# Kernel optimization log

Measured on AMD Instinct MI355X. Metric: run time of the kernel, lower is better.

Reference implementation:

```python
import jax, jax.numpy as jnp
import numpy as np
from jax import lax

HIDDEN = 1024; HEADS = 16; HEAD = 64; LAYERS = 4; MLP = 4096
PATCH = 16; TUBE = 2; CROP = 224; FRAMES = 16
GRID = CROP // PATCH          # 14
DEPTH = FRAMES // TUBE        # 8
N_TOK = DEPTH * GRID * GRID   # 1568
EPS = 1e-6
D_ROT = 2 * ((HEAD // 3) // 2)  # 20 per rotary axis (d, h, w); 4 dims left unrotated


def setup_inputs() -> dict:
    key = jax.random.key(0)
    ks = jax.random.split(key, 12)
    w = lambda k, shape: jax.random.normal(k, shape, jnp.float32) * 0.02
    L, H, M = LAYERS, HIDDEN, MLP
    return {
        "pixel_values_videos": jax.random.normal(ks[0], (2, FRAMES, 3, CROP, CROP), jnp.float32),
        "patch_w": w(ks[1], (H, 3, TUBE, PATCH, PATCH)),  # Conv3d OIDHW
        "patch_b": jnp.zeros((H,), jnp.float32),
        "ln1_g": jnp.ones((L, H), jnp.float32), "ln1_b": jnp.zeros((L, H), jnp.float32),
        "qw": w(ks[2], (L, H, H)), "qb": jnp.zeros((L, H), jnp.float32),
        "kw": w(ks[3], (L, H, H)), "kb": jnp.zeros((L, H), jnp.float32),
        "vw": w(ks[4], (L, H, H)), "vb": jnp.zeros((L, H), jnp.float32),
        "pw": w(ks[5], (L, H, H)), "pb": jnp.zeros((L, H), jnp.float32),
        "ln2_g": jnp.ones((L, H), jnp.float32), "ln2_b": jnp.zeros((L, H), jnp.float32),
        "fc1w": w(ks[6], (L, M, H)), "fc1b": jnp.zeros((L, M), jnp.float32),
        "fc2w": w(ks[7], (L, H, M)), "fc2b": jnp.zeros((L, H), jnp.float32),
        "lnf_g": jnp.ones((H,), jnp.float32), "lnf_b": jnp.zeros((H,), jnp.float32),
    }


def _layer_norm(x, g, b):
    mu = jnp.mean(x, axis=-1, keepdims=True)
    var = jnp.mean(jnp.square(x - mu), axis=-1, keepdims=True)
    return (x - mu) * lax.rsqrt(var + EPS) * g + b


def _position_ids():
    ids = jnp.arange(N_TOK)
    tpf = GRID * GRID
    d_pos = ids // tpf
    rem = ids - d_pos * tpf
    h_pos = rem // GRID
    w_pos = rem - h_pos * GRID
    return d_pos, h_pos, w_pos


def _rotate(x, pos):
    # x: (B, H, N, D); matches VJEPA2 rotate_queries_or_keys:
    # tiled (not interleaved) sin/cos * interleaved rotate-half.
    D = x.shape[-1]
    omega = 1.0 / (10000.0 ** (jnp.arange(D // 2, dtype=x.dtype) / (D / 2.0)))
    freq = pos.astype(x.dtype)[:, None] * omega              # (N, D/2)
    sin = jnp.concatenate([jnp.sin(freq)] * 2, axis=-1)      # (N, D) tiled (torch .repeat)
    cos = jnp.concatenate([jnp.cos(freq)] * 2, axis=-1)
    y = x.reshape(x.shape[:-1] + (D // 2, 2))
    y = jnp.stack([-y[..., 1], y[..., 0]], axis=-1).reshape(x.shape)
    return x * cos + y * sin


def _apply_rope(x, pos_ids):
    d_pos, h_pos, w_pos = pos_ids
    s0, s1, s2 = 0, D_ROT, 2 * D_ROT
    parts = [_rotate(x[..., s0:s1], d_pos), _rotate(x[..., s1:s2], h_pos),
             _rotate(x[..., s2:3 * D_ROT], w_pos)]
    if 3 * D_ROT < HEAD:
        parts.append(x[..., 3 * D_ROT:])
    return jnp.concatenate(parts, axis=-1)


def _forward(pixel_values_videos, patch_w, patch_b, ln1_g, ln1_b, qw, qb, kw, kb,
             vw, vb, pw, pb, ln2_g, ln2_b, fc1w, fc1b, fc2w, fc2b, lnf_g, lnf_b):
    B = pixel_values_videos.shape[0]
    x = jnp.transpose(pixel_values_videos, (0, 2, 1, 3, 4))  # (B, C, T, H, W)
    h = lax.conv_general_dilated(x, patch_w, window_strides=(TUBE, PATCH, PATCH),
                                 padding="VALID",
                                 dimension_numbers=("NCDHW", "OIDHW", "NCDHW"))
    h = h + patch_b[None, :, None, None, None]
    h = h.reshape(B, HIDDEN, -1).transpose(0, 2, 1)          # (B, N, HIDDEN)

    pos_ids = _position_ids()
    scale = HEAD ** -0.5

    for i in range(LAYERS):
        # attention block
        xn = _layer_norm(h, ln1_g[i], ln1_b[i])
        def heads(w_, b_):
            return (xn @ w_.T + b_).reshape(B, N_TOK, HEADS, HEAD).transpose(0, 2, 1, 3)
        q = _apply_rope(heads(qw[i], qb[i]), pos_ids)
        k = _apply_rope(heads(kw[i], kb[i]), pos_ids)
        v = heads(vw[i], vb[i])
        aw = jnp.einsum("bhnd,bhmd->bhnm", q, k) * scale
        aw = jax.nn.softmax(aw.astype(jnp.float32), axis=-1).astype(q.dtype)
        o = jnp.einsum("bhnm,bhmd->bhnd", aw, v)
        o = o.transpose(0, 2, 1, 3).reshape(B, N_TOK, HIDDEN)
        h = h + (o @ pw[i].T + pb[i])
        # MLP block
        xn = _layer_norm(h, ln2_g[i], ln2_b[i])
        m = jax.nn.gelu(xn @ fc1w[i].T + fc1b[i], approximate=False)
        h = h + (m @ fc2w[i].T + fc2b[i])

    return _layer_norm(h, lnf_g, lnf_b)


def reference(pixel_values_videos, patch_w, patch_b, ln1_g, ln1_b, qw, qb, kw, kb,
              vw, vb, pw, pb, ln2_g, ln2_b, fc1w, fc1b, fc2w, fc2b, lnf_g, lnf_b):
    return _forward(pixel_values_videos, patch_w, patch_b, ln1_g, ln1_b, qw, qb, kw, kb,
                    vw, vb, pw, pb, ln2_g, ln2_b, fc1w, fc1b, fc2w, fc2b, lnf_g, lnf_b)
```

## Files before the change

kernel.cpp:

```cpp
#include <hip/hip_runtime.h>
#include <math.h>

#define NTOK   1568
#define BATCH  2
#define HID    1024
#define MLPD   4096
#define NLAYER 4
#define ROWS   (BATCH*NTOK)
#define CONVK  1536

typedef __bf16 bf16x8 __attribute__((ext_vector_type(8)));
typedef __bf16 bf16x2 __attribute__((ext_vector_type(2)));
typedef float  f32x4  __attribute__((ext_vector_type(4)));

__device__ __forceinline__ unsigned short f2b(float f) {
  unsigned int u = __float_as_uint(f);
  unsigned int r = u + 0x7FFFu + ((u >> 16) & 1u);
  return (unsigned short)(r >> 16);
}
__device__ __forceinline__ float b2f(unsigned short s) {
  return __uint_as_float((unsigned int)s << 16);
}
__device__ __forceinline__ unsigned cvt2(float a, float b) {
  bf16x2 t;
  t[0] = (__bf16)a;
  t[1] = (__bf16)b;
  return __builtin_bit_cast(unsigned, t);
}
__device__ __forceinline__ float e2(float x) { return __builtin_amdgcn_exp2f(x); }

__device__ __forceinline__ void async16(const unsigned short* g, unsigned short* l) {
  __builtin_amdgcn_global_load_lds(
      (__attribute__((address_space(1))) void*)(void*)g,
      (__attribute__((address_space(3))) void*)(void*)l, 16, 0, 0);
}

__global__ __launch_bounds__(256) void cast4_k(const float* __restrict__ s,
                                               unsigned short* __restrict__ d,
                                               long long n4) {
  long long i = (long long)blockIdx.x * 256 + threadIdx.x;
  long long stride = (long long)gridDim.x * 256;
  for (; i < n4; i += stride) {
    float4 v = ((const float4*)s)[i];
    *(ushort4*)(d + i * 4) = make_ushort4(f2b(v.x), f2b(v.y), f2b(v.z), f2b(v.w));
  }
}

__global__ __launch_bounds__(256) void castqkv_k(const float* __restrict__ q,
                                                 const float* __restrict__ k,
                                                 const float* __restrict__ v,
                                                 unsigned short* __restrict__ dst) {
  const float* src = blockIdx.y == 0 ? q : (blockIdx.y == 1 ? k : v);
  long long i4 = (long long)blockIdx.x * 256 + threadIdx.x;
  long long e = i4 * 4;
  int layer = (int)(e >> 20);
  long long de = e + ((long long)(2 * layer + blockIdx.y) << 20);
  float4 val = ((const float4*)src)[i4];
  *(ushort4*)(dst + de) = make_ushort4(f2b(val.x), f2b(val.y), f2b(val.z), f2b(val.w));
}

__global__ __launch_bounds__(256) void biascat_k(const float* __restrict__ qb,
                                                 const float* __restrict__ kb,
                                                 const float* __restrict__ vb,
                                                 float* __restrict__ dst) {
  int idx = blockIdx.x * 256 + threadIdx.x;
  int layer = idx / 3072, c = idx % 3072;
  float v = c < 1024 ? qb[layer * 1024 + c]
            : (c < 2048 ? kb[layer * 1024 + c - 1024] : vb[layer * 1024 + c - 2048]);
  dst[idx] = v;
}

__global__ __launch_bounds__(256) void im2col_k(const float* __restrict__ pv,
                                                unsigned short* __restrict__ A) {
  int idx = blockIdx.x * 256 + threadIdx.x;
  int row = idx / CONVK, col = idx % CONVK;
  int b = row / NTOK, t = row % NTOK;
  int d = t / 196, r = t % 196, hh = r / 14, ww = r % 14;
  int c = col >> 9, r2 = col & 511, td = r2 >> 8, ph = (r2 >> 4) & 15, pw = r2 & 15;
  int frame = 2 * d + td;
  const float* src = pv + ((((long long)b * 16 + frame) * 3 + c) * 224 + (hh * 16 + ph)) * 224
                        + (ww * 16 + pw);
  A[idx] = f2b(*src);
}

__global__ __launch_bounds__(256) void gemm_bt(const unsigned short* __restrict__ A,
                                               const unsigned short* __restrict__ B,
                                               unsigned short* outP,
                                               int M, int N, int K, int kChunk,
                                               size_t zStride) {
  __shared__ unsigned short As[3][128 * 32];
  __shared__ unsigned short Bs[3][128 * 32];
  const int tid = threadIdx.x;
  const int lane = tid & 63;
  const int w = tid >> 6;
  const int wm = (w >> 1) * 64, wn = (w & 1) * 64;
  const int l15 = lane & 15, l4 = lane >> 4;
  const int bm = blockIdx.y, bn = blockIdx.x;
  const int wbase = tid & ~63;
  const int kbeg = blockIdx.z * kChunk;

  auto stage = [&](int buf, int k0) {
#pragma unroll
    for (int it = 0; it < 2; ++it) {
      int c = it * 256 + tid;
      int row = c >> 2;
      int sc = (c & 3) ^ ((row >> 1) & 3);
      int rowA = bm * 128 + row;
      if (rowA >= M) rowA = M - 1;
      async16(A + (size_t)rowA * K + k0 + sc * 8, &As[buf][(it * 256 + wbase) * 8]);
      int rowB = bn * 128 + row;
      async16(B + (size_t)rowB * K + k0 + sc * 8, &Bs[buf][(it * 256 + wbase) * 8]);
    }
  };

  f32x4 acc[4][4] = {};
  const int nIter = kChunk >> 5;

  stage(0, kbeg);
  stage(1, kbeg + 32);

  const int pchunk = (l4 ^ ((l15 >> 1) & 3)) * 8;

  int cur = 0, pre = 2;
  for (int i = 0; i < nIter; ++i) {
    if (i + 1 < nIter) {
      asm volatile("s_waitcnt vmcnt(4)" ::: "memory");
    } else {
      asm volatile("s_waitcnt vmcnt(0)" ::: "memory");
    }
    __builtin_amdgcn_s_barrier();
    __builtin_amdgcn_sched_barrier(0);
    if (i + 2 < nIter) stage(pre, kbeg + (i + 2) * 32);

    bf16x8 af[4], bfr[4];
#pragma unroll
    for (int ii = 0; ii < 4; ++ii)
      af[ii] = *(const bf16x8*)&As[cur][(wm + ii * 16 + l15) * 32 + pchunk];
#pragma unroll
    for (int j = 0; j < 4; ++j)
      bfr[j] = *(const bf16x8*)&Bs[cur][(wn + j * 16 + l15) * 32 + pchunk];
    __builtin_amdgcn_s_setprio(1);
#pragma unroll
    for (int ii = 0; ii < 4; ++ii)
#pragma unroll
      for (int j = 0; j < 4; ++j)
        acc[ii][j] = __builtin_amdgcn_mfma_f32_16x16x32_bf16(af[ii], bfr[j], acc[ii][j], 0, 0, 0);
    __builtin_amdgcn_s_setprio(0);
    __builtin_amdgcn_sched_barrier(0);
    cur = cur == 2 ? 0 : cur + 1;
    pre = pre == 2 ? 0 : pre + 1;
  }

  unsigned short* pout = outP + (size_t)blockIdx.z * zStride;
#pragma unroll
  for (int ii = 0; ii < 4; ++ii) {
    int rowb = bm * 128 + wm + ii * 16 + l4 * 4;
#pragma unroll
    for (int r = 0; r < 4; ++r) {
      int rr = rowb + r;
      if (rr >= M) continue;
#pragma unroll
      for (int j = 0; j < 4; ++j) {
        int col = bn * 128 + wn + j * 16 + l15;
        pout[(size_t)rr * N + col] = f2b(acc[ii][j][r]);
      }
    }
  }
}

template <int NP, int GELU>
__global__ __launch_bounds__(256) void reduceN_k(const unsigned short* p,
                                                 const float* __restrict__ bias,
                                                 unsigned short* outB,
                                                 int MN, int N, size_t pStride) {
  int i8 = blockIdx.x * 256 + threadIdx.x;
  int e = i8 * 8;
  float acc[8];
#pragma unroll
  for (int j = 0; j < 8; ++j) acc[j] = 0.0f;
#pragma unroll
  for (int pp = 0; pp < NP; ++pp) {
    const unsigned short* src = p + (size_t)pp * pStride + e;
    ushort4 a0 = *(const ushort4*)src;
    ushort4 a1 = *(const ushort4*)(src + 4);
    acc[0] += b2f(a0.x); acc[1] += b2f(a0.y); acc[2] += b2f(a0.z); acc[3] += b2f(a0.w);
    acc[4] += b2f(a1.x); acc[5] += b2f(a1.y); acc[6] += b2f(a1.z); acc[7] += b2f(a1.w);
  }
  int col = e % N;
  float4 b0 = *(const float4*)(bias + col);
  float4 b1 = *(const float4*)(bias + col + 4);
  acc[0] += b0.x; acc[1] += b0.y; acc[2] += b0.z; acc[3] += b0.w;
  acc[4] += b1.x; acc[5] += b1.y; acc[6] += b1.z; acc[7] += b1.w;
  if (GELU) {
#pragma unroll
    for (int j = 0; j < 8; ++j)
      acc[j] = 0.5f * acc[j] * (1.0f + erff(acc[j] * 0.70710678118654752f));
  }
  *(ushort4*)(outB + e) = make_ushort4(f2b(acc[0]), f2b(acc[1]), f2b(acc[2]), f2b(acc[3]));
  *(ushort4*)(outB + e + 4) = make_ushort4(f2b(acc[4]), f2b(acc[5]), f2b(acc[6]), f2b(acc[7]));
}

template <int NP, int RESID, int FINAL>
__global__ __launch_bounds__(256) void redln_k(const unsigned short* __restrict__ p,
                                               const float* __restrict__ bias,
                                               const float* resid,
                                               const float* __restrict__ g,
                                               const float* __restrict__ b,
                                               float* hOut,
                                               unsigned short* __restrict__ xnOut,
                                               float* __restrict__ fOut,
                                               size_t pStride) {
  __shared__ float red[8];
  const int row = blockIdx.x, tid = threadIdx.x;
  const int col = tid * 4;
  const size_t off = (size_t)row * HID + col;
  float v0 = 0, v1 = 0, v2 = 0, v3 = 0;
#pragma unroll
  for (int pp = 0; pp < NP; ++pp) {
    ushort4 a = *(const ushort4*)(p + (size_t)pp * pStride + off);
    v0 += b2f(a.x); v1 += b2f(a.y); v2 += b2f(a.z); v3 += b2f(a.w);
  }
  float4 bs = *(const float4*)(bias + col);
  v0 += bs.x; v1 += bs.y; v2 += bs.z; v3 += bs.w;
  if (RESID) {
    float4 r = *(const float4*)(resid + off);
    v0 += r.x; v1 += r.y; v2 += r.z; v3 += r.w;
  }
  if (!FINAL) *(float4*)(hOut + off) = make_float4(v0, v1, v2, v3);
  float s = v0 + v1 + v2 + v3;
  float q = v0 * v0 + v1 * v1 + v2 * v2 + v3 * v3;
  for (int o2 = 32; o2; o2 >>= 1) { s += __shfl_xor(s, o2); q += __shfl_xor(q, o2); }
  if ((tid & 63) == 0) { red[tid >> 6] = s; red[4 + (tid >> 6)] = q; }
  __syncthreads();
  float ts = red[0] + red[1] + red[2] + red[3];
  float tq = red[4] + red[5] + red[6] + red[7];
  float mu = ts * (1.0f / HID);
  float var = tq * (1.0f / HID) - mu * mu;
  float rs = rsqrtf(var + 1e-6f);
  float o0 = (v0 - mu) * rs * g[col + 0] + b[col + 0];
  float o1 = (v1 - mu) * rs * g[col + 1] + b[col + 1];
  float o2 = (v2 - mu) * rs * g[col + 2] + b[col + 2];
  float o3 = (v3 - mu) * rs * g[col + 3] + b[col + 3];
  if (FINAL) {
    *(float4*)(fOut + off) = make_float4(o0, o1, o2, o3);
  } else {
    *(ushort4*)(xnOut + off) = make_ushort4(f2b(o0), f2b(o1), f2b(o2), f2b(o3));
  }
}

__global__ __launch_bounds__(256) void qkvprep_k(const unsigned short* __restrict__ qkvb,
                                                 unsigned short* __restrict__ Qh,
                                                 unsigned short* __restrict__ Kh,
                                                 unsigned short* __restrict__ VT) {
  __shared__ unsigned short Vs[64 * 72];
  const int tile = blockIdx.x, bh = blockIdx.y;
  const int b = bh >> 4, head = bh & 15;
  const int tid = threadIdx.x;
  const int tl = tid >> 2, dc = tid & 3;
  const int tg = tile * 64 + tl;
  const int trc = tg < NTOK ? tg : NTOK - 1;
  const bool valid = tg < NTOK;
  const size_t srow = ((size_t)(b * NTOK + trc)) * 3072 + head * 64 + dc * 16;

  {
    uint4 v0 = *(const uint4*)(qkvb + srow + 2048);
    uint4 v1 = *(const uint4*)(qkvb + srow + 2048 + 8);
    *(uint4*)&Vs[tl * 72 + dc * 16] = v0;
    *(uint4*)&Vs[tl * 72 + dc * 16 + 8] = v1;
  }

  const int t = trc;
  const int dpos = t / 196, rem = t - dpos * 196, hpos = rem / 14, wpos = rem - hpos * 14;
  const float LG = 0.9210340371976184f;
  union V16 { uint4 u[2]; unsigned short s[16]; };
  V16 qin, kin, qout, kout;
  qin.u[0] = *(const uint4*)(qkvb + srow);
  qin.u[1] = *(const uint4*)(qkvb + srow + 8);
  kin.u[0] = *(const uint4*)(qkvb + srow + 1024);
  kin.u[1] = *(const uint4*)(qkvb + srow + 1024 + 8);
#pragma unroll
  for (int p = 0; p < 8; ++p) {
    int d0 = dc * 16 + 2 * p;
    float qx0 = b2f(qin.s[2 * p]), qx1 = b2f(qin.s[2 * p + 1]);
    float kx0 = b2f(kin.s[2 * p]), kx1 = b2f(kin.s[2 * p + 1]);
    float qo0, qo1, ko0, ko1;
    if (d0 >= 60) { qo0 = qx0; qo1 = qx1; ko0 = kx0; ko1 = kx1; }
    else {
      int region = d0 / 20;
      int j0 = d0 - region * 20;
      int pos = region == 0 ? dpos : (region == 1 ? hpos : wpos);
      float fp = (float)pos;
      int i0 = j0 % 10, i1 = (j0 + 1) % 10;
      float f0 = expf(-LG * (float)i0) * fp;
      float f1 = expf(-LG * (float)i1) * fp;
      float c0 = cosf(f0), s0 = sinf(f0), c1 = cosf(f1), s1 = sinf(f1);
      qo0 = qx0 * c0 - qx1 * s0; qo1 = qx1 * c1 + qx0 * s1;
      ko0 = kx0 * c0 - kx1 * s0; ko1 = kx1 * c1 + kx0 * s1;
    }
    const float QS = 0.18033688011112042f;
    qout.s[2 * p]     = f2b(qo0 * QS);
    qout.s[2 * p + 1] = f2b(qo1 * QS);
    kout.s[2 * p]     = f2b(ko0);
    kout.s[2 * p + 1] = f2b(ko1);
  }
  if (valid) {
    size_t drow = ((size_t)bh * NTOK + tg) * 64 + dc * 16;
    *(uint4*)(Qh + drow)     = qout.u[0];
    *(uint4*)(Qh + drow + 8) = qout.u[1];
    *(uint4*)(Kh + drow)     = kout.u[0];
    *(uint4*)(Kh + drow + 8) = kout.u[1];
  }
  __syncthreads();
  {
    int d = tid >> 2, tc = tid & 3;
    if (tile * 64 + tc * 16 < NTOK) {
      V16 o;
#pragma unroll
      for (int jj = 0; jj < 16; ++jj) o.s[jj] = Vs[(tc * 16 + jj) * 72 + d];
      unsigned short* dst = VT + ((size_t)bh * 64 + d) * NTOK + tile * 64 + tc * 16;
      *(uint4*)dst = o.u[0];
      *(uint4*)(dst + 8) = o.u[1];
    }
  }
}

__global__ __launch_bounds__(256, 4) void flash5_k(const unsigned short* __restrict__ Qh,
                                                   const unsigned short* __restrict__ Kh,
                                                   const unsigned short* __restrict__ VT,
                                                   unsigned short* __restrict__ Opart,
                                                   float2* __restrict__ ml) {
  __shared__ unsigned short Ks[2][64 * 64];
  __shared__ unsigned short Vs[2][64 * 64];
  const int bh = blockIdx.x, qt = blockIdx.y, kv = blockIdx.z;
  const int kt0 = kv ? 13 : 0, kt1 = kv ? 25 : 13;
  const int tid = threadIdx.x, lane = tid & 63, w = tid >> 6;
  const int l15 = lane & 15, l4 = lane >> 4;
  const size_t hb = (size_t)bh * NTOK * 64;
  const unsigned short* kgp = Kh + hb;
  const unsigned short* vbp = VT + (size_t)bh * 64 * NTOK;

  const int srow0 = w * 8 + (lane >> 3);
  const int scg0  = (lane & 7) ^ (srow0 & 7);
  const int srow1 = srow0 + 32;
  const int scg1  = (lane & 7) ^ (srow1 & 7);

  const int qrow = qt * 64 + w * 16 + l15;
  const int qrc = qrow < NTOK ? qrow : NTOK - 1;
  bf16x8 q0 = *(const bf16x8*)(Qh + hb + (size_t)qrc * 64 + l4 * 8);
  bf16x8 q1 = *(const bf16x8*)(Qh + hb + (size_t)qrc * 64 + 32 + l4 * 8);

  f32x4 oacc[4] = {};
  float m = -1e30f, l = 0.0f;

  {
    const int kc0 = kt0 * 64;
    async16(kgp + (size_t)(kc0 + srow0) * 64 + scg0 * 8, &Ks[0][(size_t)w * 512]);
    async16(kgp + (size_t)(kc0 + srow1) * 64 + scg1 * 8, &Ks[0][(size_t)(w + 4) * 512]);
    async16(vbp + (size_t)srow0 * NTOK + kc0 + scg0 * 8, &Vs[0][(size_t)w * 512]);
    async16(vbp + (size_t)srow1 * NTOK + kc0 + scg1 * 8, &Vs[0][(size_t)(w + 4) * 512]);
  }

  const int h7 = l15 & 7;
  const int p1 = (l4 ^ h7) * 8;
  const int p2 = ((l4 + 4) ^ h7) * 8;

  for (int kt = kt0; kt < kt1; ++kt) {
    const int cur = (kt - kt0) & 1, nxt = cur ^ 1;
    const int kb = kt * 64;
    __syncthreads();

    if (kt + 1 < kt1) {
      const int kn = kb + 64;
      async16(kgp + (size_t)(kn + srow0) * 64 + scg0 * 8, &Ks[nxt][(size_t)w * 512]);
      async16(kgp + (size_t)(kn + srow1) * 64 + scg1 * 8, &Ks[nxt][(size_t)(w + 4) * 512]);
      async16(vbp + (size_t)srow0 * NTOK + kn + scg0 * 8, &Vs[nxt][(size_t)w * 512]);
      async16(vbp + (size_t)srow1 * NTOK + kn + scg1 * 8, &Vs[nxt][(size_t)(w + 4) * 512]);
    }

    bf16x8 kc0[4], kc1[4];
#pragma unroll
    for (int nt = 0; nt < 4; ++nt) {
      const unsigned short* kr = &Ks[cur][(nt * 16 + l15) * 64];
      kc0[nt] = *(const bf16x8*)(kr + p1);
      kc1[nt] = *(const bf16x8*)(kr + p2);
    }
    f32x4 s[4] = {};
    __builtin_amdgcn_s_setprio(1);
#pragma unroll
    for (int nt = 0; nt < 4; ++nt) {
      s[nt] = __builtin_amdgcn_mfma_f32_16x16x32_bf16(kc0[nt], q0, s[nt], 0, 0, 0);
      s[nt] = __builtin_amdgcn_mfma_f32_16x16x32_bf16(kc1[nt], q1, s[nt], 0, 0, 0);
    }
    __builtin_amdgcn_s_setprio(0);
    bf16x8 vf0[4], vf1[4];
#pragma unroll
    for (int dt = 0; dt < 4; ++dt) {
      const unsigned short* vr = &Vs[cur][(dt * 16 + l15) * 64];
      vf0[dt] = *(const bf16x8*)(vr + p1);
      vf1[dt] = *(const bf16x8*)(vr + p2);
    }

    if (kb + 64 > NTOK) {
#pragma unroll
      for (int nt = 0; nt < 4; ++nt)
#pragma unroll
        for (int r = 0; r < 4; ++r)
          if (kb + nt * 16 + l4 * 4 + r >= NTOK) s[nt][r] = -1e30f;
    }
    float rmax = s[0][0];
#pragma unroll
    for (int nt = 0; nt < 4; ++nt)
#pragma unroll
      for (int r = 0; r < 4; ++r) rmax = fmaxf(rmax, s[nt][r]);
    rmax = fmaxf(rmax, __shfl_xor(rmax, 16));
    rmax = fmaxf(rmax, __shfl_xor(rmax, 32));
    if (!__all(rmax - m <= 11.5f)) {
      float mn = fmaxf(m, rmax);
      float alpha = e2(m - mn);
      m = mn;
      l *= alpha;
#pragma unroll
      for (int dt = 0; dt < 4; ++dt)
#pragma unroll
        for (int r = 0; r < 4; ++r) oacc[dt][r] *= alpha;
    }
    float rsum = 0.0f;
#pragma unroll
    for (int nt = 0; nt < 4; ++nt)
#pragma unroll
      for (int r = 0; r < 4; ++r) {
        float p = e2(s[nt][r] - m);
        s[nt][r] = p;
        rsum += p;
      }
    rsum += __shfl_xor(rsum, 16);
    rsum += __shfl_xor(rsum, 32);
    l += rsum;

    unsigned pk01[4], pk23[4];
#pragma unroll
    for (int nt = 0; nt < 4; ++nt) {
      pk01[nt] = cvt2(s[nt][0], s[nt][1]);
      pk23[nt] = cvt2(s[nt][2], s[nt][3]);
    }
    const int srcA = ((l4 & 1) << 5) | l15;
    const int srcB = srcA + 16;
    const bool hi = (l4 >> 1) != 0;
    union PB { unsigned u[4]; bf16x8 v; } pf[2];
#pragma unroll
    for (int kc = 0; kc < 2; ++kc) {
      unsigned t0, t1;
      t0 = __shfl(pk01[2 * kc], srcA); t1 = __shfl(pk01[2 * kc + 1], srcA);
      pf[kc].u[0] = hi ? t1 : t0;
      t0 = __shfl(pk23[2 * kc], srcA); t1 = __shfl(pk23[2 * kc + 1], srcA);
      pf[kc].u[1] = hi ? t1 : t0;
      t0 = __shfl(pk01[2 * kc], srcB); t1 = __shfl(pk01[2 * kc + 1], srcB);
      pf[kc].u[2] = hi ? t1 : t0;
      t0 = __shfl(pk23[2 * kc], srcB); t1 = __shfl(pk23[2 * kc + 1], srcB);
      pf[kc].u[3] = hi ? t1 : t0;
    }
    __builtin_amdgcn_s_setprio(1);
#pragma unroll
    for (int dt = 0; dt < 4; ++dt) {
      oacc[dt] = __builtin_amdgcn_mfma_f32_16x16x32_bf16(vf0[dt], pf[0].v, oacc[dt], 0, 0, 0);
      oacc[dt] = __builtin_amdgcn_mfma_f32_16x16x32_bf16(vf1[dt], pf[1].v, oacc[dt], 0, 0, 0);
    }
    __builtin_amdgcn_s_setprio(0);
  }

  __syncthreads();
  unsigned short* Os = &Ks[0][0];
#pragma unroll
  for (int dt = 0; dt < 4; ++dt)
#pragma unroll
    for (int r = 0; r < 4; ++r)
      Os[w * 1152 + l15 * 72 + dt * 16 + l4 * 4 + r] = f2b(oacc[dt][r]);
  if (qrow < NTOK) {
    uint4 a  = *(const uint4*)&Os[w * 1152 + l15 * 72 + l4 * 16];
    uint4 bq = *(const uint4*)&Os[w * 1152 + l15 * 72 + l4 * 16 + 8];
    unsigned short* op = Opart + ((size_t)(kv * 32 + bh) * NTOK + qrow) * 64;
    *(uint4*)(op + l4 * 16) = a;
    *(uint4*)(op + l4 * 16 + 8) = bq;
    if (l4 == 0) ml[(size_t)(kv * 32 + bh) * NTOK + qrow] = make_float2(m, l);
  }
}

__global__ __launch_bounds__(256) void fcomb_k(const unsigned short* __restrict__ Op,
                                               const float2* __restrict__ ml,
                                               unsigned short* __restrict__ O) {
  const int bh = blockIdx.x, qt = blockIdx.y;
  const int tid = threadIdx.x;
  const int qr = qt * 64 + (tid >> 2);
  const int dc = (tid & 3) * 16;
  if (qr >= NTOK) return;
  const int b = bh >> 4, head = bh & 15;
  float2 a0 = ml[(size_t)bh * NTOK + qr];
  float2 a1 = ml[(size_t)(32 + bh) * NTOK + qr];
  float M = fmaxf(a0.x, a1.x);
  float w0 = e2(a0.x - M), w1 = e2(a1.x - M);
  float inv = 1.0f / (a0.y * w0 + a1.y * w1);
  w0 *= inv; w1 *= inv;
  union V16 { uint4 u[2]; unsigned short s[16]; } p0, p1, o;
  const unsigned short* q0 = Op + ((size_t)bh * NTOK + qr) * 64 + dc;
  const unsigned short* q1 = Op + ((size_t)(32 + bh) * NTOK + qr) * 64 + dc;
  p0.u[0] = *(const uint4*)q0;       p0.u[1] = *(const uint4*)(q0 + 8);
  p1.u[0] = *(const uint4*)q1;       p1.u[1] = *(const uint4*)(q1 + 8);
#pragma unroll
  for (int j = 0; j < 16; ++j) o.s[j] = f2b(b2f(p0.s[j]) * w0 + b2f(p1.s[j]) * w1);
  unsigned short* dst = O + ((size_t)(b * NTOK + qr)) * HID + head * 64 + dc;
  *(uint4*)dst = o.u[0];
  *(uint4*)(dst + 8) = o.u[1];
}

extern "C" void kernel_launch(void* const* d_in, const int* in_sizes, int n_in,
                              void* d_out, int out_size, void* d_ws, size_t ws_size,
                              hipStream_t stream) {
  (void)in_sizes; (void)n_in; (void)out_size; (void)ws_size;
  const float* pv      = (const float*)d_in[0];
  const float* patch_w = (const float*)d_in[1];
  const float* patch_b = (const float*)d_in[2];
  const float* ln1_g   = (const float*)d_in[3];
  const float* ln1_b   = (const float*)d_in[4];
  const float* qw = (const float*)d_in[5];
  const float* qb = (const float*)d_in[6];
  const float* kw = (const float*)d_in[7];
  const float* kb = (const float*)d_in[8];
  const float* vw = (const float*)d_in[9];
  const float* vb = (const float*)d_in[10];
  const float* pw = (const float*)d_in[11];
  const float* pb = (const float*)d_in[12];
  const float* ln2_g = (const float*)d_in[13];
  const float* ln2_b = (const float*)d_in[14];
  const float* fc1w = (const float*)d_in[15];
  const float* fc1b = (const float*)d_in[16];
  const float* fc2w = (const float*)d_in[17];
  const float* fc2b = (const float*)d_in[18];
  const float* lnf_g = (const float*)d_in[19];
  const float* lnf_b = (const float*)d_in[20];

  char* wsp = (char*)d_ws;
  auto alloc = [&](size_t bytes) {
    char* p = wsp;
    wsp += (bytes + 255) & ~(size_t)255;
    return p;
  };
  unsigned short* wPatch = (unsigned short*)alloc((size_t)1024 * 1536 * 2);
  unsigned short* wQKV   = (unsigned short*)alloc((size_t)NLAYER * 3072 * 1024 * 2);
  unsigned short* wP     = (unsigned short*)alloc((size_t)NLAYER * HID * HID * 2);
  unsigned short* wF1    = (unsigned short*)alloc((size_t)NLAYER * MLPD * HID * 2);
  unsigned short* wF2    = (unsigned short*)alloc((size_t)NLAYER * HID * MLPD * 2);
  float*          qkvbias = (float*)alloc((size_t)NLAYER * 3072 * 4);
  unsigned short* Aim  = (unsigned short*)alloc((size_t)ROWS * CONVK * 2);
  float*          h    = (float*)alloc((size_t)ROWS * HID * 4);
  unsigned short* xnb  = (unsigned short*)alloc((size_t)ROWS * HID * 2);
  unsigned short* qkvo = (unsigned short*)alloc((size_t)ROWS * 3072 * 2);
  unsigned short* Qh   = (unsigned short*)alloc((size_t)ROWS * HID * 2 + 8192);
  unsigned short* Kh   = (unsigned short*)alloc((size_t)ROWS * HID * 2 + 8192);
  unsigned short* VT   = (unsigned short*)alloc((size_t)ROWS * HID * 2 + 8192);
  unsigned short* ob   = (unsigned short*)alloc((size_t)ROWS * HID * 2);
  unsigned short* mb   = (unsigned short*)alloc((size_t)ROWS * MLPD * 2);

  unsigned short* part  = Qh;
  unsigned short* partM = mb;
  unsigned short* Opart = mb;
  float2*         mlbuf = (float2*)(mb + (size_t)2 * 32 * NTOK * 64);
  const size_t MNs = (size_t)ROWS * HID;
  const size_t strideF1 = (size_t)(mb - part);

  auto cast = [&](const float* s, unsigned short* d, long long n) {
    long long n4 = n / 4;
    int grid = (int)((n4 + 255) / 256);
    if (grid > 16384) grid = 16384;
    cast4_k<<<grid, 256, 0, stream>>>(s, d, n4);
  };
  cast(patch_w, wPatch, (long long)1024 * 1536);
  castqkv_k<<<dim3(4096, 3), 256, 0, stream>>>(qw, kw, vw, wQKV);
  cast(pw, wP, (long long)NLAYER * HID * HID);
  cast(fc1w, wF1, (long long)NLAYER * MLPD * HID);
  cast(fc2w, wF2, (long long)NLAYER * HID * MLPD);
  biascat_k<<<48, 256, 0, stream>>>(qb, kb, vb, qkvbias);

  im2col_k<<<(ROWS * CONVK) / 256, 256, 0, stream>>>(pv, Aim);
  gemm_bt<<<dim3(8, 25, 3), 256, 0, stream>>>(Aim, wPatch, part, ROWS, HID, CONVK, 512, MNs);
  redln_k<3, 0, 0><<<ROWS, 256, 0, stream>>>(
      part, patch_b, nullptr, ln1_g, ln1_b, h, xnb, nullptr, MNs);

  for (int i = 0; i < NLAYER; ++i) {
    gemm_bt<<<dim3(24, 25, 2), 256, 0, stream>>>(
        xnb, wQKV + (size_t)i * 3072 * 1024, part, ROWS, 3072, HID, 512,
        (size_t)ROWS * 3072);
    reduceN_k<2, 0><<<(ROWS * 3072) / 2048, 256, 0, stream>>>(
        part, qkvbias + i * 3072, qkvo, ROWS * 3072, 3072, (size_t)ROWS * 3072);
    qkvprep_k<<<dim3(25, 32), 256, 0, stream>>>(qkvo, Qh, Kh, VT);
    flash5_k<<<dim3(32, 25, 2), 256, 0, stream>>>(Qh, Kh, VT, Opart, mlbuf);
    fcomb_k<<<dim3(32, 25), 256, 0, stream>>>(Opart, mlbuf, ob);
    gemm_bt<<<dim3(8, 25, 4), 256, 0, stream>>>(
        ob, wP + (size_t)i * HID * HID, partM, ROWS, HID, HID, 256, MNs);
    redln_k<4, 1, 0><<<ROWS, 256, 0, stream>>>(
        partM, pb + i * HID, h, ln2_g + i * HID, ln2_b + i * HID, h, xnb, nullptr, MNs);
    gemm_bt<<<dim3(32, 25, 2), 256, 0, stream>>>(
        xnb, wF1 + (size_t)i * MLPD * HID, part, ROWS, MLPD, HID, 512, strideF1);
    reduceN_k<2, 1><<<(ROWS * MLPD) / 2048, 256, 0, stream>>>(
        part, fc1b + i * MLPD, mb, ROWS * MLPD, MLPD, strideF1);
    gemm_bt<<<dim3(8, 25, 4), 256, 0, stream>>>(
        mb, wF2 + (size_t)i * HID * MLPD, part, ROWS, HID, MLPD, 1024, MNs);
    if (i < NLAYER - 1) {
      redln_k<4, 1, 0><<<ROWS, 256, 0, stream>>>(
          part, fc2b + i * HID, h, ln1_g + (i + 1) * HID, ln1_b + (i + 1) * HID,
          h, xnb, nullptr, MNs);
    } else {
      redln_k<4, 1, 1><<<ROWS, 256, 0, stream>>>(
          part, fc2b + i * HID, h, lnf_g, lnf_b, nullptr, nullptr, (float*)d_out, MNs);
    }
  }
}
```

Before: 1.392 ms.

## Replace 128x128 GEMM with 256x256-tile 512-thread kernel and XCD-aware block swizzle

Swaps the 128x128-tile, 256-thread GEMM for a 256x256-tile, 512-thread kernel with 8 waves, each owning a 128x64 sub-tile. The A and B prefetches are split around two MFMA half-phases. Block indices are remapped so consecutive tiles land on the same XCD, and split-K is reduced or removed for the QKV and FC1 GEMMs, which shrinks the partial-sum reduction traffic. The larger tiles cut global and LDS traffic per FLOP, but they mean fewer workgroups (e.g. 156 for QKV), which risks underfilling the 256 CUs and adds register pressure.

```diff
diff --git a/kernel.cpp b/kernel.cpp
--- a/kernel.cpp
+++ b/kernel.cpp
@@ -83,86 +83,122 @@
   A[idx] = f2b(*src);
 }
 
-__global__ __launch_bounds__(256) void gemm_bt(const unsigned short* __restrict__ A,
-                                               const unsigned short* __restrict__ B,
-                                               unsigned short* outP,
-                                               int M, int N, int K, int kChunk,
-                                               size_t zStride) {
-  __shared__ unsigned short As[3][128 * 32];
-  __shared__ unsigned short Bs[3][128 * 32];
+__global__ __launch_bounds__(512, 2) void gemm256(const unsigned short* __restrict__ A,
+                                                  const unsigned short* __restrict__ B,
+                                                  unsigned short* outP,
+                                                  int M, int N, int K, int kChunk,
+                                                  size_t zStride) {
+  __shared__ unsigned short As[3][256 * 32];
+  __shared__ unsigned short Bs[3][256 * 32];
   const int tid = threadIdx.x;
   const int lane = tid & 63;
   const int w = tid >> 6;
-  const int wm = (w >> 1) * 64, wn = (w & 1) * 64;
+  const int wr = w >> 2, wc = w & 3;
   const int l15 = lane & 15, l4 = lane >> 4;
-  const int bm = blockIdx.y, bn = blockIdx.x;
   const int wbase = tid & ~63;
-  const int kbeg = blockIdx.z * kChunk;
-
-  auto stage = [&](int buf, int k0) {
-#pragma unroll
-    for (int it = 0; it < 2; ++it) {
-      int c = it * 256 + tid;
-      int row = c >> 2;
-      int sc = (c & 3) ^ ((row >> 1) & 3);
-      int rowA = bm * 128 + row;
-      if (rowA >= M) rowA = M - 1;
-      async16(A + (size_t)rowA * K + k0 + sc * 8, &As[buf][(it * 256 + wbase) * 8]);
-      int rowB = bn * 128 + row;
-      async16(B + (size_t)rowB * K + k0 + sc * 8, &Bs[buf][(it * 256 + wbase) * 8]);
-    }
+
+  const int gx = gridDim.x, gy = gridDim.y;
+  const int nwg = gx * gy * (int)gridDim.z;
+  int orig = blockIdx.x + gx * (blockIdx.y + gy * blockIdx.z);
+  int q = nwg >> 3, r = nwg & 7, xcd = orig & 7, idx = orig >> 3;
+  int swz = (xcd < r ? xcd * (q + 1) : r * (q + 1) + (xcd - r) * q) + idx;
+  const int bn = swz % gx;
+  int tmp = swz / gx;
+  const int bm = tmp % gy;
+  const int bz = tmp / gy;
+  const int kbeg = bz * kChunk;
+
+  const int r0 = tid >> 2;
+  const int g0 = (tid & 3) ^ ((tid >> 3) & 3);
+  const int i1 = 512 + tid;
+  const int r1 = i1 >> 2;
+  const int g1 = (tid & 3) ^ ((i1 >> 3) & 3);
+  int ra0 = bm * 256 + r0; if (ra0 >= M) ra0 = M - 1;
+  int ra1 = bm * 256 + r1; if (ra1 >= M) ra1 = M - 1;
+  const int rb0 = bn * 256 + r0;
+  const int rb1 = bn * 256 + r1;
+  const size_t Ao0 = (size_t)ra0 * K + g0 * 8;
+  const size_t Ao1 = (size_t)ra1 * K + g1 * 8;
+  const size_t Bo0 = (size_t)rb0 * K + g0 * 8;
+  const size_t Bo1 = (size_t)rb1 * K + g1 * 8;
+
+  auto stA = [&](int buf, int k0) {
+    async16(A + Ao0 + k0, &As[buf][wbase * 8]);
+    async16(A + Ao1 + k0, &As[buf][4096 + wbase * 8]);
   };
-
-  f32x4 acc[4][4] = {};
-  const int nIter = kChunk >> 5;
-
-  stage(0, kbeg);
-  stage(1, kbeg + 32);
+  auto stB = [&](int buf, int k0) {
+    async16(B + Bo0 + k0, &Bs[buf][wbase * 8]);
+    async16(B + Bo1 + k0, &Bs[buf][4096 + wbase * 8]);
+  };
+
+  f32x4 acc[8][4] = {};
+  const int nk = kChunk >> 5;
+
+  stA(0, kbeg); stB(0, kbeg);
+  stA(1, kbeg + 32); stB(1, kbeg + 32);
 
   const int pchunk = (l4 ^ ((l15 >> 1) & 3)) * 8;
-
-  int cur = 0, pre = 2;
-  for (int i = 0; i < nIter; ++i) {
-    if (i + 1 < nIter) {
+  const int abase = (wr * 128 + l15) * 32 + pchunk;
+  const int bbase = (wc * 64 + l15) * 32 + pchunk;
+
+  int cur = 0;
+  for (int kt = 0; kt < nk; ++kt) {
+    if (kt + 1 < nk) {
       asm volatile("s_waitcnt vmcnt(4)" ::: "memory");
     } else {
       asm volatile("s_waitcnt vmcnt(0)" ::: "memory");
     }
     __builtin_amdgcn_s_barrier();
     __builtin_amdgcn_sched_barrier(0);
-    if (i + 2 < nIter) stage(pre, kbeg + (i + 2) * 32);
-
-    bf16x8 af[4], bfr[4];
-#pragma unroll
-    for (int ii = 0; ii < 4; ++ii)
-      af[ii] = *(const bf16x8*)&As[cur][(wm + ii * 16 + l15) * 32 + pchunk];
-#pragma unroll
-    for (int j = 0; j < 4; ++j)
-      bfr[j] = *(const bf16x8*)&Bs[cur][(wn + j * 16 + l15) * 32 + pchunk];
+    const int prebuf = cur >= 1 ? cur - 1 : 2;
+    const bool doPre = (kt + 2 < nk);
+    const int kpre = kbeg + (kt + 2) * 32;
+
+    if (doPre) stA(prebuf, kpre);
+    bf16x8 bfr[4], af[4];
+#pragma unroll
+    for (int n = 0; n < 4; ++n)
+      bfr[n] = *(const bf16x8*)&Bs[cur][bbase + n * 512];
+#pragma unroll
+    for (int m = 0; m < 4; ++m)
+      af[m] = *(const bf16x8*)&As[cur][abase + m * 512];
     __builtin_amdgcn_s_setprio(1);
 #pragma unroll
-    for (int ii = 0; ii < 4; ++ii)
-#pragma unroll
-      for (int j = 0; j < 4; ++j)
-        acc[ii][j] = __builtin_amdgcn_mfma_f32_16x16x32_bf16(af[ii], bfr[j], acc[ii][j], 0, 0, 0);
+    for (int m = 0; m < 4; ++m)
+#pragma unroll
+      for (int n = 0; n < 4; ++n)
+        acc[m][n] = __builtin_amdgcn_mfma_f32_16x16x32_bf16(af[m], bfr[n], acc[m][n], 0, 0, 0);
     __builtin_amdgcn_s_setprio(0);
     __builtin_amdgcn_sched_barrier(0);
+
+    if (doPre) stB(prebuf, kpre);
+#pragma unroll
+    for (int m = 0; m < 4; ++m)
+      af[m] = *(const bf16x8*)&As[cur][abase + (m + 4) * 512];
+    __builtin_amdgcn_s_setprio(1);
+#pragma unroll
+    for (int m = 0; m < 4; ++m)
+#pragma unroll
+      for (int n = 0; n < 4; ++n)
+        acc[m + 4][n] = __builtin_amdgcn_mfma_f32_16x16x32_bf16(af[m], bfr[n], acc[m + 4][n], 0, 0, 0);
+    __builtin_amdgcn_s_setprio(0);
+    __builtin_amdgcn_sched_barrier(0);
+
     cur = cur == 2 ? 0 : cur + 1;
-    pre = pre == 2 ? 0 : pre + 1;
-  }
-
-  unsigned short* pout = outP + (size_t)blockIdx.z * zStride;
-#pragma unroll
-  for (int ii = 0; ii < 4; ++ii) {
-    int rowb = bm * 128 + wm + ii * 16 + l4 * 4;
-#pragma unroll
-    for (int r = 0; r < 4; ++r) {
-      int rr = rowb + r;
+  }
+
+  unsigned short* pout = outP + (size_t)bz * zStride;
+#pragma unroll
+  for (int m = 0; m < 8; ++m) {
+    int rowb = bm * 256 + wr * 128 + m * 16 + l4 * 4;
+#pragma unroll
+    for (int rr2 = 0; rr2 < 4; ++rr2) {
+      int rr = rowb + rr2;
       if (rr >= M) continue;
 #pragma unroll
-      for (int j = 0; j < 4; ++j) {
-        int col = bn * 128 + wn + j * 16 + l15;
-        pout[(size_t)rr * N + col] = f2b(acc[ii][j][r]);
+      for (int n = 0; n < 4; ++n) {
+        int col = bn * 256 + wc * 64 + n * 16 + l15;
+        pout[(size_t)rr * N + col] = f2b(acc[m][n][rr2]);
       }
     }
   }
@@ -565,7 +601,6 @@
   unsigned short* Opart = mb;
   float2*         mlbuf = (float2*)(mb + (size_t)2 * 32 * NTOK * 64);
   const size_t MNs = (size_t)ROWS * HID;
-  const size_t strideF1 = (size_t)(mb - part);
 
   auto cast = [&](const float* s, unsigned short* d, long long n) {
     long long n4 = n / 4;
@@ -581,28 +616,28 @@
   biascat_k<<<48, 256, 0, stream>>>(qb, kb, vb, qkvbias);
 
   im2col_k<<<(ROWS * CONVK) / 256, 256, 0, stream>>>(pv, Aim);
-  gemm_bt<<<dim3(8, 25, 3), 256, 0, stream>>>(Aim, wPatch, part, ROWS, HID, CONVK, 512, MNs);
-  redln_k<3, 0, 0><<<ROWS, 256, 0, stream>>>(
+  gemm256<<<dim3(4, 13, 4), 512, 0, stream>>>(Aim, wPatch, part, ROWS, HID, CONVK, 384, MNs);
+  redln_k<4, 0, 0><<<ROWS, 256, 0, stream>>>(
       part, patch_b, nullptr, ln1_g, ln1_b, h, xnb, nullptr, MNs);
 
   for (int i = 0; i < NLAYER; ++i) {
-    gemm_bt<<<dim3(24, 25, 2), 256, 0, stream>>>(
-        xnb, wQKV + (size_t)i * 3072 * 1024, part, ROWS, 3072, HID, 512,
+    gemm256<<<dim3(12, 13, 1), 512, 0, stream>>>(
+        xnb, wQKV + (size_t)i * 3072 * 1024, part, ROWS, 3072, HID, 1024,
         (size_t)ROWS * 3072);
-    reduceN_k<2, 0><<<(ROWS * 3072) / 2048, 256, 0, stream>>>(
+    reduceN_k<1, 0><<<(ROWS * 3072) / 2048, 256, 0, stream>>>(
         part, qkvbias + i * 3072, qkvo, ROWS * 3072, 3072, (size_t)ROWS * 3072);
     qkvprep_k<<<dim3(25, 32), 256, 0, stream>>>(qkvo, Qh, Kh, VT);
     flash5_k<<<dim3(32, 25, 2), 256, 0, stream>>>(Qh, Kh, VT, Opart, mlbuf);
     fcomb_k<<<dim3(32, 25), 256, 0, stream>>>(Opart, mlbuf, ob);
-    gemm_bt<<<dim3(8, 25, 4), 256, 0, stream>>>(
+    gemm256<<<dim3(4, 13, 4), 512, 0, stream>>>(
         ob, wP + (size_t)i * HID * HID, partM, ROWS, HID, HID, 256, MNs);
     redln_k<4, 1, 0><<<ROWS, 256, 0, stream>>>(
         partM, pb + i * HID, h, ln2_g + i * HID, ln2_b + i * HID, h, xnb, nullptr, MNs);
-    gemm_bt<<<dim3(32, 25, 2), 256, 0, stream>>>(
-        xnb, wF1 + (size_t)i * MLPD * HID, part, ROWS, MLPD, HID, 512, strideF1);
-    reduceN_k<2, 1><<<(ROWS * MLPD) / 2048, 256, 0, stream>>>(
-        part, fc1b + i * MLPD, mb, ROWS * MLPD, MLPD, strideF1);
-    gemm_bt<<<dim3(8, 25, 4), 256, 0, stream>>>(
+    gemm256<<<dim3(16, 13, 1), 512, 0, stream>>>(
+        xnb, wF1 + (size_t)i * MLPD * HID, part, ROWS, MLPD, HID, 1024, MNs);
+    reduceN_k<1, 1><<<(ROWS * MLPD) / 2048, 256, 0, stream>>>(
+        part, fc1b + i * MLPD, mb, ROWS * MLPD, MLPD, MNs);
+    gemm256<<<dim3(4, 13, 4), 512, 0, stream>>>(
         mb, wF2 + (size_t)i * HID * MLPD, part, ROWS, HID, MLPD, 1024, MNs);
     if (i < NLAYER - 1) {
       redln_k<4, 1, 0><<<ROWS, 256, 0, stream>>>(
```

After: 1.305 ms. 1.07x faster.
